# Kernel optimization log

Hardware: AMD Instinct MI355X
Metric: run time of the kernel (lower is better)

The kernel has to match this reference:

```python
import jax, jax.numpy as jnp
jax.config.update("jax_enable_x64", True)
import numpy as np

B, S, BITS = 1024, 4096, 32
_SHIFTS = jnp.arange(31, -1, -1, dtype=jnp.uint32)  # bit 0 = MSB


def _decode_fp32(bits):
    """[..., 32] {0,1} pulses -> float32 values (bitwise-exact)."""
    u = jnp.sum(bits.astype(jnp.uint32) << _SHIFTS, axis=-1, dtype=jnp.uint32)
    return jax.lax.bitcast_convert_type(u, jnp.float32)


def _encode_fp32(vals):
    """float32 values -> [..., 32] {0,1} pulses (bitwise-exact)."""
    u = jax.lax.bitcast_convert_type(vals, jnp.uint32)
    return ((u[..., None] >> _SHIFTS) & jnp.uint32(1)).astype(jnp.float32)


def _gelu_exact_fp64(x32):
    """Mirror of the spiking pipeline: fp32->fp64, exact tanh-GELU in fp64
    using tanh(z) = (exp(2z)-1)/(exp(2z)+1), then round back to fp32."""
    x = x32.astype(jnp.float64)                      # FP32ToFP64Converter
    x_cubed = (x * x) * x                            # two fp64 muls
    inner = x + 0.044715 * x_cubed                   # adder + mul
    two_z = 2.0 * (0.7978845608028654 * inner)       # two muls
    e = jnp.exp(two_z)                               # fp64 exp
    tanh = (e - 1.0) / (e + 1.0)                     # adders + divider
    y = 0.5 * (x * (1.0 + tanh))                     # adder + two muls
    return y.astype(jnp.float32)                     # FP64ToFP32Converter


def setup_inputs() -> dict:
    key = jax.random.key(0)
    # Generate realistic pre-activation values and bit-expand to pulses so the
    # [..., 32] pulse tensor encodes valid IEEE-754 float32 patterns.
    vals = jax.random.normal(key, (B, S), dtype=jnp.float32) * 2.0
    return {"x": _encode_fp32(vals)}


def reference(x) -> jnp.ndarray:
    # x: [B, S, 32] pulse bits -> GELU(x) as [B, S, 32] pulse bits
    return _encode_fp32(_gelu_exact_fp64(_decode_fp32(x)))
```

## Files before the change

kernel.cpp:

```cpp
#include <hip/hip_runtime.h>
#include <cmath>


__global__ __launch_bounds__(256) void spike_gelu_kernel(
    const float4* __restrict__ in, float4* __restrict__ out, long n4) {
  long f = (long)blockIdx.x * (long)blockDim.x + (long)threadIdx.x;
  if (f >= n4) return;

  float4 p = in[f];

  unsigned g = (unsigned)threadIdx.x & 7u;
  unsigned nib = ((p.x != 0.0f) ? 8u : 0u) | ((p.y != 0.0f) ? 4u : 0u) |
                 ((p.z != 0.0f) ? 2u : 0u) | ((p.w != 0.0f) ? 1u : 0u);
  unsigned s = 28u - 4u * g;
  unsigned u = nib << s;

  u |= __shfl_xor(u, 1, 8);
  u |= __shfl_xor(u, 2, 8);
  u |= __shfl_xor(u, 4, 8);

  float xf = __uint_as_float(u);

  double y;
  {
#pragma clang fp contract(off)
    double x = (double)xf;
    double x_cubed = (x * x) * x;
    double inner = x + 0.044715 * x_cubed;
    double two_z = 2.0 * (0.7978845608028654 * inner);
    double e = exp(two_z);
    double th = (e - 1.0) / (e + 1.0);
    y = 0.5 * (x * (1.0 + th));
  }
  float yf = (float)y;

  unsigned r = __float_as_uint(yf);
  float4 o;
  o.x = (float)((r >> (s + 3u)) & 1u);
  o.y = (float)((r >> (s + 2u)) & 1u);
  o.z = (float)((r >> (s + 1u)) & 1u);
  o.w = (float)((r >> s) & 1u);
  out[f] = o;
}

extern "C" void kernel_launch(void* const* d_in, const int* in_sizes, int n_in,
                              void* d_out, int out_size, void* d_ws, size_t ws_size,
                              hipStream_t stream) {
  const float4* in = (const float4*)d_in[0];
  float4* out = (float4*)d_out;
  long n4 = (long)in_sizes[0] / 4;
  int block = 256;
  long grid = (n4 + block - 1) / block;
  spike_gelu_kernel<<<(int)grid, block, 0, stream>>>(in, out, n4);
}
```

Measured before the change: 802.6 us.

## Compute each GELU value once per lane using wave-level shuffle redistribution

Previously the 8 threads sharing one 32-bit value each ran the full fp64 GELU, so the fp64 exp and divide were done 8 times per value. Now each wave loads 512 float4s in 8 coalesced rounds and assembles the 32-bit words with xor-shuffles. It then routes one distinct value to each lane, so every lane computes exactly one GELU. Results are shuffled back out to write the bit pulses. This cuts redundant fp64 arithmetic 8x, at the cost of more cross-lane shuffles and more registers per thread.

```diff
diff --git a/kernel.cpp b/kernel.cpp
--- a/kernel.cpp
+++ b/kernel.cpp
@@ -4,22 +4,33 @@
 
 __global__ __launch_bounds__(256) void spike_gelu_kernel(
     const float4* __restrict__ in, float4* __restrict__ out, long n4) {
-  long f = (long)blockIdx.x * (long)blockDim.x + (long)threadIdx.x;
-  if (f >= n4) return;
+  const unsigned l = threadIdx.x & 63u;
+  const long wave_id = (((long)blockIdx.x * blockDim.x) + threadIdx.x) >> 6;
+  const long fbase = wave_id * 512;
+  if (fbase >= n4) return;
 
-  float4 p = in[f];
+  const unsigned g = l & 7u;
+  const unsigned s = 28u - 4u * g;
+  const unsigned kown = l >> 3;
+  const unsigned src_in = (l & 7u) << 3;
 
-  unsigned g = (unsigned)threadIdx.x & 7u;
-  unsigned nib = ((p.x != 0.0f) ? 8u : 0u) | ((p.y != 0.0f) ? 4u : 0u) |
-                 ((p.z != 0.0f) ? 2u : 0u) | ((p.w != 0.0f) ? 1u : 0u);
-  unsigned s = 28u - 4u * g;
-  unsigned u = nib << s;
+  unsigned myu = 0u;
+#pragma unroll
+  for (unsigned k = 0; k < 8; ++k) {
+    long fi = fbase + (long)(k * 64u + l);
+    if (fi >= n4) fi = n4 - 1;
+    float4 p = in[fi];
+    unsigned nib = ((p.x != 0.0f) ? 8u : 0u) | ((p.y != 0.0f) ? 4u : 0u) |
+                   ((p.z != 0.0f) ? 2u : 0u) | ((p.w != 0.0f) ? 1u : 0u);
+    unsigned u = nib << s;
+    u |= __shfl_xor(u, 1, 8);
+    u |= __shfl_xor(u, 2, 8);
+    u |= __shfl_xor(u, 4, 8);
+    unsigned t = __shfl(u, (int)src_in, 64);
+    if (kown == k) myu = t;
+  }
 
-  u |= __shfl_xor(u, 1, 8);
-  u |= __shfl_xor(u, 2, 8);
-  u |= __shfl_xor(u, 4, 8);
-
-  float xf = __uint_as_float(u);
+  float xf = __uint_as_float(myu);
 
   double y;
   {
@@ -32,15 +43,19 @@
     double th = (e - 1.0) / (e + 1.0);
     y = 0.5 * (x * (1.0 + th));
   }
-  float yf = (float)y;
+  unsigned r = __float_as_uint((float)y);
 
-  unsigned r = __float_as_uint(yf);
-  float4 o;
-  o.x = (float)((r >> (s + 3u)) & 1u);
-  o.y = (float)((r >> (s + 2u)) & 1u);
-  o.z = (float)((r >> (s + 1u)) & 1u);
-  o.w = (float)((r >> s) & 1u);
-  out[f] = o;
+#pragma unroll
+  for (unsigned k = 0; k < 8; ++k) {
+    unsigned w = __shfl(r, (int)((k << 3) + kown), 64);
+    float4 o;
+    o.x = (float)((w >> (s + 3u)) & 1u);
+    o.y = (float)((w >> (s + 2u)) & 1u);
+    o.z = (float)((w >> (s + 1u)) & 1u);
+    o.w = (float)((w >> s) & 1u);
+    long fi = fbase + (long)(k * 64u + l);
+    if (fi < n4) out[fi] = o;
+  }
 }
 
 extern "C" void kernel_launch(void* const* d_in, const int* in_sizes, int n_in,
@@ -49,7 +64,8 @@
   const float4* in = (const float4*)d_in[0];
   float4* out = (float4*)d_out;
   long n4 = (long)in_sizes[0] / 4;
+  long nvals = n4 / 8;
   int block = 256;
-  long grid = (n4 + block - 1) / block;
+  long grid = (nvals + block - 1) / block;
   spike_gelu_kernel<<<(int)grid, block, 0, stream>>>(in, out, n4);
 }
```

After: 837.5 us. 4.3% more time.
